# Kernel optimization log

Measured on AMD Instinct MI355X. Metric: run time of the kernel, lower is better.

## Reference

```python
import jax, jax.numpy as jnp
import numpy as np

SEQ = 4096
R_DIM = 1024
Z_DIM = 1024
AT_DIM = 1024
G_DIM = 1024


def _xavier(key, shape):
    fan_in, fan_out = shape[1], shape[0]
    limit = float(np.sqrt(6.0 / (fan_in + fan_out)))
    return jax.random.uniform(key, shape, jnp.float32, -limit, limit)


def setup_inputs() -> dict:
    key = jax.random.key(0)
    ks = jax.random.split(key, 12)
    return {
        "R": jax.random.normal(ks[0], (SEQ, R_DIM), jnp.float32),
        "W_alpha": _xavier(ks[1], (R_DIM, 2 * R_DIM)),
        "b_alpha": jnp.zeros((R_DIM,), jnp.float32),
        "W_delta": _xavier(ks[2], (R_DIM, 2 * R_DIM)),
        "b_delta": jnp.zeros((R_DIM,), jnp.float32),
        "W_q": _xavier(ks[3], (AT_DIM, Z_DIM)),
        "b_q": jnp.zeros((AT_DIM,), jnp.float32),
        "W_k": _xavier(ks[4], (AT_DIM, Z_DIM)),
        "b_k": jnp.zeros((AT_DIM,), jnp.float32),
        "W_v": _xavier(ks[5], (AT_DIM, Z_DIM)),
        "b_v": jnp.zeros((AT_DIM,), jnp.float32),
        "W_z": _xavier(ks[6], (Z_DIM, R_DIM)),
        "b_z": jnp.zeros((Z_DIM,), jnp.float32),
        "W_f": _xavier(ks[7], (AT_DIM, G_DIM)),
        "b_f": jnp.zeros((AT_DIM,), jnp.float32),
        "W_EMA": _xavier(ks[8], (G_DIM, R_DIM)),
        "b_EMA": jnp.zeros((G_DIM,), jnp.float32),
        "W_z_at": _xavier(ks[9], (G_DIM, AT_DIM)),
        "b_z_at": jnp.zeros((G_DIM,), jnp.float32),
        "W_i": _xavier(ks[10], (1, R_DIM)),
        "b_i": jnp.zeros((1,), jnp.float32),
        "W_final": _xavier(ks[11], (1, G_DIM)),
    }


def reference(R, W_alpha, b_alpha, W_delta, b_delta, W_q, b_q, W_k, b_k,
              W_v, b_v, W_z, b_z, W_f, b_f, W_EMA, b_EMA, W_z_at, b_z_at,
              W_i, b_i, W_final):
    r_dim = R.shape[-1]
    at_dim = W_q.shape[0]
    # prepend zero row; r_t / r_{t-1} pairs
    R2 = jnp.concatenate([jnp.zeros((1, r_dim), R.dtype), R], axis=0)
    r_t, r_prev = R2[1:], R2[:-1]
    concat_r = jnp.concatenate([r_prev, r_t], axis=1)  # [m, 2r]
    alpha = jnp.tanh(concat_r @ W_alpha.T + b_alpha)
    delta = jnp.tanh(concat_r @ W_delta.T + b_delta)
    R_EMA = alpha * r_t + (1.0 - alpha) * delta * r_prev
    Z = jax.nn.silu(R_EMA @ W_z.T + b_z)
    Q = Z @ W_q.T + b_q
    K = Z @ W_k.T + b_k
    V = Z @ W_v.T + b_v
    scores = (Q @ K.T) / jnp.sqrt(jnp.float32(at_dim))  # [m, m]
    weights = jax.nn.softmax(scores, axis=-1)
    Z_at = weights @ V
    R_EMA_p = R_EMA @ W_EMA.T + b_EMA
    f = jax.nn.sigmoid(R_EMA_p @ W_f.T + b_f)
    Z_at_p = f * Z_at
    Z_EMA_f = Z_at_p @ W_z_at.T + b_z_at
    Z_tp = jnp.tanh(R_EMA_p + Z_EMA_f)
    i = jnp.tanh(R_EMA @ W_i.T + b_i)  # [m, 1]
    Z_final = i * Z_tp + (1.0 - i) * R_EMA_p
    p_hat = jax.nn.sigmoid(Z_final @ W_final.T)  # [m, 1]
    return p_hat
```

## Files before the change

kernel.cpp:

```cpp
#include <hip/hip_runtime.h>
#include <cstdint>
#include <cmath>

#define MB (1024ull * 1024ull)

typedef unsigned short u16;
typedef __attribute__((ext_vector_type(8))) short short8;
typedef __attribute__((ext_vector_type(4))) float f32x4;

enum { M_TANH = 0, M_ZRE = 1, M_QKV = 2, M_SIG = 3, M_SCALE = 4, M_PVMUL = 5, M_F32 = 6 };

__device__ __forceinline__ u16 f2b(float f) {
  union { float f; uint32_t u; } v; v.f = f;
  uint32_t r = v.u + 0x7FFFu + ((v.u >> 16) & 1u);
  return (u16)(r >> 16);
}
__device__ __forceinline__ float b2f(u16 u) {
  union { uint32_t u; float f; } v; v.u = ((uint32_t)u) << 16;
  return v.f;
}

typedef __attribute__((address_space(3))) uint32_t lds_u32;
typedef const __attribute__((address_space(1))) uint32_t glb_u32;

__device__ __forceinline__ void gload16(const void* g, void* l) {
  __builtin_amdgcn_global_load_lds((glb_u32*)g, (lds_u32*)l, 16, 0, 0);
}

template <int MODE, int BNT>
__global__ __launch_bounds__(256) void gemm(const u16* __restrict__ A,
                                            const u16* __restrict__ B,
                                            const float* __restrict__ bias,
                                            const u16* __restrict__ auxb,
                                            u16* __restrict__ Cb,
                                            u16* __restrict__ Cb2,
                                            float* __restrict__ Cf,
                                            int K, int lda, int ldb, float scale) {
  constexpr int NJ = (BNT == 128) ? 4 : 2;
  __shared__ u16 As[128 * 32];
  __shared__ u16 Bs[BNT * 32];
  const int tid = threadIdx.x;
  const int wid = tid >> 6, lane = tid & 63;
  const int bm = blockIdx.y * 128, bn = blockIdx.x * BNT;
  const int wm = wid >> 1, wn = wid & 1;

  const int srow = tid >> 2;
  const int schunk = (tid & 3) ^ ((srow >> 1) & 3);
  const u16* gA = A + (size_t)(bm + srow) * lda + schunk * 8;
  const u16* gB = B + (size_t)(bn + srow) * ldb + schunk * 8;
  u16* ldsA = &As[wid * 512];
  u16* ldsB = &Bs[wid * 512];

  f32x4 acc[4][NJ];
#pragma unroll
  for (int i = 0; i < 4; ++i)
#pragma unroll
    for (int j = 0; j < NJ; ++j) acc[i][j] = (f32x4){0.f, 0.f, 0.f, 0.f};

  const int ar = lane & 15;
  const int pch = (((lane >> 4) ^ ((ar >> 1) & 3))) * 8;

  for (int k0 = 0; k0 < K; k0 += 32) {
    gload16(gA, ldsA);
    gload16(gA + (size_t)64 * lda, ldsA + 2048);
    gload16(gB, ldsB);
    if (BNT == 128) gload16(gB + (size_t)64 * ldb, ldsB + 2048);
    gA += 32; gB += 32;
    __syncthreads();
    short8 af[4], bf[NJ];
#pragma unroll
    for (int i = 0; i < 4; ++i)
      af[i] = *reinterpret_cast<const short8*>(&As[(wm * 64 + i * 16 + ar) * 32 + pch]);
#pragma unroll
    for (int j = 0; j < NJ; ++j)
      bf[j] = *reinterpret_cast<const short8*>(&Bs[(wn * (BNT / 2) + j * 16 + ar) * 32 + pch]);
#pragma unroll
    for (int i = 0; i < 4; ++i)
#pragma unroll
      for (int j = 0; j < NJ; ++j)
        acc[i][j] = __builtin_amdgcn_mfma_f32_16x16x32_bf16(af[i], bf[j], acc[i][j], 0, 0, 0);
    __syncthreads();
  }

#pragma unroll
  for (int i = 0; i < 4; ++i) {
    const int rb = bm + wm * 64 + i * 16 + (lane >> 4) * 4;
#pragma unroll
    for (int j = 0; j < NJ; ++j) {
      const int n = bn + wn * (BNT / 2) + j * 16 + (lane & 15);
#pragma unroll
      for (int r = 0; r < 4; ++r) {
        const int m = rb + r;
        float v = acc[i][j][r];
        if (MODE == M_TANH) {
          v = tanhf(v + bias[n]);
          Cb[(size_t)m * 2048 + n] = f2b(v);
        } else if (MODE == M_ZRE) {
          v += bias[n];
          if (n < 1024) { const float s = v / (1.f + expf(-v)); Cb[(size_t)m * 1024 + n] = f2b(s); }
          else Cb2[(size_t)m * 1024 + (n - 1024)] = f2b(v);
        } else if (MODE == M_QKV) {
          v += bias[n];
          if (n < 2048) Cb[(size_t)m * 2048 + n] = f2b(v);
          else Cb2[(size_t)m * 1024 + (n - 2048)] = f2b(v);
        } else if (MODE == M_SIG) {
          v = 1.f / (1.f + expf(-(v + bias[n])));
          Cb[(size_t)m * 1024 + n] = f2b(v);
        } else if (MODE == M_SCALE) {
          Cb[(size_t)m * 4096 + n] = f2b(v * scale);
        } else if (MODE == M_PVMUL) {
          v *= b2f(auxb[(size_t)m * 1024 + n]);
          Cb[(size_t)m * 1024 + n] = f2b(v);
        } else if (MODE == M_F32) {
          Cf[(size_t)m * 1024 + n] = v + bias[n];
        }
      }
    }
  }
}

__global__ __launch_bounds__(256) void convert_all(
    const float* __restrict__ s0, const float* __restrict__ s1, const float* __restrict__ s2,
    const float* __restrict__ s3, const float* __restrict__ s4, const float* __restrict__ s5,
    const float* __restrict__ s6, const float* __restrict__ s7, const float* __restrict__ s8,
    u16* __restrict__ Wad, u16* __restrict__ Wze, u16* __restrict__ Wqkv,
    u16* __restrict__ Wfb, u16* __restrict__ Wzab) {
  const int idx = blockIdx.x * 256 + threadIdx.x;
  const float* src; u16* dst; int off;
  if      (idx < 524288)  { src = s0; dst = Wad;           off = idx; }
  else if (idx < 1048576) { src = s1; dst = Wad + 2097152; off = idx - 524288; }
  else if (idx < 1310720) { src = s2; dst = Wze;           off = idx - 1048576; }
  else if (idx < 1572864) { src = s3; dst = Wze + 1048576; off = idx - 1310720; }
  else if (idx < 1835008) { src = s4; dst = Wqkv;          off = idx - 1572864; }
  else if (idx < 2097152) { src = s5; dst = Wqkv + 1048576; off = idx - 1835008; }
  else if (idx < 2359296) { src = s6; dst = Wqkv + 2097152; off = idx - 2097152; }
  else if (idx < 2621440) { src = s7; dst = Wfb;           off = idx - 2359296; }
  else                    { src = s8; dst = Wzab;          off = idx - 2621440; }
  const float4 v = reinterpret_cast<const float4*>(src)[off];
  ushort4 o; o.x = f2b(v.x); o.y = f2b(v.y); o.z = f2b(v.z); o.w = f2b(v.w);
  reinterpret_cast<ushort4*>(dst)[off] = o;
}

__global__ void copy_bias(const float* __restrict__ ba, const float* __restrict__ bd,
                          const float* __restrict__ bz, const float* __restrict__ be,
                          const float* __restrict__ bq, const float* __restrict__ bk,
                          const float* __restrict__ bv,
                          float* __restrict__ bad, float* __restrict__ bze,
                          float* __restrict__ bqkv) {
  const int t = threadIdx.x;
  const float4* src; float4* dst;
  switch (blockIdx.x) {
    case 0: src = (const float4*)ba; dst = (float4*)bad; break;
    case 1: src = (const float4*)bd; dst = (float4*)(bad + 1024); break;
    case 2: src = (const float4*)bz; dst = (float4*)bze; break;
    case 3: src = (const float4*)be; dst = (float4*)(bze + 1024); break;
    case 4: src = (const float4*)bq; dst = (float4*)bqkv; break;
    case 5: src = (const float4*)bk; dst = (float4*)(bqkv + 1024); break;
    default: src = (const float4*)bv; dst = (float4*)(bqkv + 2048); break;
  }
  dst[t] = src[t];
}

__global__ __launch_bounds__(256) void concat_kern(const float* __restrict__ R,
                                                   u16* __restrict__ Rc) {
  const int idx = blockIdx.x * 256 + threadIdx.x;
  const int m = idx >> 9;
  const int c = (idx & 511) * 4;
  float4 v;
  if (c < 1024) {
    if (m > 0) v = *reinterpret_cast<const float4*>(&R[(size_t)(m - 1) * 1024 + c]);
    else v = make_float4(0.f, 0.f, 0.f, 0.f);
  } else {
    v = *reinterpret_cast<const float4*>(&R[(size_t)m * 1024 + (c - 1024)]);
  }
  ushort4 o; o.x = f2b(v.x); o.y = f2b(v.y); o.z = f2b(v.z); o.w = f2b(v.w);
  reinterpret_cast<ushort4*>(Rc)[idx] = o;
}

__global__ __launch_bounds__(256) void ema_combine(const float* __restrict__ R,
                                                   const u16* __restrict__ adb,
                                                   u16* __restrict__ REMA) {
  const int idx = blockIdx.x * 256 + threadIdx.x;
  const int m = idx >> 8, c4 = idx & 255;
  const float4 rt = reinterpret_cast<const float4*>(R)[idx];
  float4 rp = make_float4(0.f, 0.f, 0.f, 0.f);
  if (m > 0) rp = reinterpret_cast<const float4*>(R)[idx - 256];
  const ushort4 a4 = reinterpret_cast<const ushort4*>(adb)[m * 512 + c4];
  const ushort4 d4 = reinterpret_cast<const ushort4*>(adb)[m * 512 + 256 + c4];
  ushort4 o;
  { const float av = b2f(a4.x); o.x = f2b(av * rt.x + (1.f - av) * b2f(d4.x) * rp.x); }
  { const float av = b2f(a4.y); o.y = f2b(av * rt.y + (1.f - av) * b2f(d4.y) * rp.y); }
  { const float av = b2f(a4.z); o.z = f2b(av * rt.z + (1.f - av) * b2f(d4.z) * rp.z); }
  { const float av = b2f(a4.w); o.w = f2b(av * rt.w + (1.f - av) * b2f(d4.w) * rp.w); }
  reinterpret_cast<ushort4*>(REMA)[idx] = o;
}

__device__ __forceinline__ float waveMax(float v) {
#pragma unroll
  for (int o = 32; o; o >>= 1) v = fmaxf(v, __shfl_down(v, o));
  return v;
}
__device__ __forceinline__ float waveSum(float v) {
#pragma unroll
  for (int o = 32; o; o >>= 1) v += __shfl_down(v, o);
  return v;
}

__global__ __launch_bounds__(256) void softmax_rows(u16* __restrict__ S) {
  u16* p = S + (size_t)blockIdx.x * 4096;
  const int tid = threadIdx.x;
  float v[16];
#pragma unroll
  for (int j = 0; j < 4; ++j) {
    const ushort4 t = *reinterpret_cast<const ushort4*>(&p[tid * 4 + 1024 * j]);
    v[4 * j + 0] = b2f(t.x); v[4 * j + 1] = b2f(t.y);
    v[4 * j + 2] = b2f(t.z); v[4 * j + 3] = b2f(t.w);
  }
  float mx = -INFINITY;
#pragma unroll
  for (int j = 0; j < 16; ++j) mx = fmaxf(mx, v[j]);
  __shared__ float red[4];
  const float wm = waveMax(mx);
  if ((tid & 63) == 0) red[tid >> 6] = wm;
  __syncthreads();
  mx = fmaxf(fmaxf(red[0], red[1]), fmaxf(red[2], red[3]));
  __syncthreads();
  float sum = 0.f;
#pragma unroll
  for (int j = 0; j < 16; ++j) { v[j] = expf(v[j] - mx); sum += v[j]; }
  const float ws_ = waveSum(sum);
  if ((tid & 63) == 0) red[tid >> 6] = ws_;
  __syncthreads();
  const float inv = 1.f / (red[0] + red[1] + red[2] + red[3]);
#pragma unroll
  for (int j = 0; j < 4; ++j) {
    ushort4 t;
    t.x = f2b(v[4 * j + 0] * inv); t.y = f2b(v[4 * j + 1] * inv);
    t.z = f2b(v[4 * j + 2] * inv); t.w = f2b(v[4 * j + 3] * inv);
    *reinterpret_cast<ushort4*>(&p[tid * 4 + 1024 * j]) = t;
  }
}

__global__ __launch_bounds__(256) void transpose_b16(const u16* __restrict__ V,
                                                     u16* __restrict__ Vt) {
  __shared__ u16 t[64][72];
  const int bn = blockIdx.x * 64;
  const int bk = blockIdx.y * 64;
  const int tx = threadIdx.x & 15, ty = threadIdx.x >> 4;
#pragma unroll
  for (int i = 0; i < 64; i += 16) {
    const ushort4 v = *reinterpret_cast<const ushort4*>(&V[(size_t)(bk + ty + i) * 1024 + bn + tx * 4]);
    t[ty + i][tx * 4 + 0] = v.x; t[ty + i][tx * 4 + 1] = v.y;
    t[ty + i][tx * 4 + 2] = v.z; t[ty + i][tx * 4 + 3] = v.w;
  }
  __syncthreads();
#pragma unroll
  for (int i = 0; i < 64; i += 16) {
    ushort4 w;
    w.x = t[tx * 4 + 0][ty + i]; w.y = t[tx * 4 + 1][ty + i];
    w.z = t[tx * 4 + 2][ty + i]; w.w = t[tx * 4 + 3][ty + i];
    *reinterpret_cast<ushort4*>(&Vt[(size_t)(bn + ty + i) * 4096 + bk + tx * 4]) = w;
  }
}

__global__ void rowdot_i(const u16* __restrict__ REMA, const float* __restrict__ Wi,
                         const float* __restrict__ bi, float* __restrict__ iv) {
  const int m = blockIdx.x, l = threadIdx.x;
  float s = 0.f;
#pragma unroll
  for (int j = 0; j < 16; ++j) s += b2f(REMA[(size_t)m * 1024 + l + 64 * j]) * Wi[l + 64 * j];
#pragma unroll
  for (int o = 32; o; o >>= 1) s += __shfl_down(s, o);
  if (l == 0) iv[m] = tanhf(s + bi[0]);
}

__global__ void final_kern(const u16* __restrict__ REMApb, const float* __restrict__ ZEMAf,
                           const float* __restrict__ iv, const float* __restrict__ Wfin,
                           float* __restrict__ out) {
  const int m = blockIdx.x, l = threadIdx.x;
  const float im = iv[m];
  float s = 0.f;
#pragma unroll
  for (int j = 0; j < 16; ++j) {
    const int n = l + 64 * j;
    const float rp = b2f(REMApb[(size_t)m * 1024 + n]);
    const float zf = im * tanhf(rp + ZEMAf[(size_t)m * 1024 + n]) + (1.f - im) * rp;
    s += zf * Wfin[n];
  }
#pragma unroll
  for (int o = 32; o; o >>= 1) s += __shfl_down(s, o);
  if (l == 0) out[m] = 1.f / (1.f + expf(-s));
}

extern "C" void kernel_launch(void* const* d_in, const int* in_sizes, int n_in,
                              void* d_out, int out_size, void* d_ws, size_t ws_size,
                              hipStream_t stream) {
  const float* R       = (const float*)d_in[0];
  const float* W_alpha = (const float*)d_in[1];  const float* b_alpha = (const float*)d_in[2];
  const float* W_delta = (const float*)d_in[3];  const float* b_delta = (const float*)d_in[4];
  const float* W_q     = (const float*)d_in[5];  const float* b_q     = (const float*)d_in[6];
  const float* W_k     = (const float*)d_in[7];  const float* b_k     = (const float*)d_in[8];
  const float* W_v     = (const float*)d_in[9];  const float* b_v     = (const float*)d_in[10];
  const float* W_z     = (const float*)d_in[11]; const float* b_z     = (const float*)d_in[12];
  const float* W_f     = (const float*)d_in[13]; const float* b_f     = (const float*)d_in[14];
  const float* W_EMA   = (const float*)d_in[15]; const float* b_EMA   = (const float*)d_in[16];
  const float* W_z_at  = (const float*)d_in[17]; const float* b_z_at  = (const float*)d_in[18];
  const float* W_i     = (const float*)d_in[19]; const float* b_i     = (const float*)d_in[20];
  const float* W_final = (const float*)d_in[21];
  float* out = (float*)d_out;
  uint8_t* w8 = (uint8_t*)d_ws;

  u16*   Rc     = (u16*)(w8 + 0 * MB);
  u16*   Zb     = (u16*)(w8 + 0 * MB);
  u16*   REMApb = (u16*)(w8 + 8 * MB);
  u16*   Wad    = (u16*)(w8 + 16 * MB);
  u16*   fvb    = (u16*)(w8 + 16 * MB);
  u16*   adb    = (u16*)(w8 + 24 * MB);
  float* ZEMAf  = (float*)(w8 + 24 * MB);
  u16*   Wqkv   = (u16*)(w8 + 40 * MB);
  u16*   Vtb    = (u16*)(w8 + 40 * MB);
  u16*   Wze    = (u16*)(w8 + 46 * MB);
  u16*   Wfb    = (u16*)(w8 + 50 * MB);
  u16*   Wzab   = (u16*)(w8 + 52 * MB);
  u16*   REMAb  = (u16*)(w8 + 54 * MB);
  u16*   QKb    = (u16*)(w8 + 62 * MB);
  u16*   Zatpb  = (u16*)(w8 + 62 * MB);
  u16*   Vb     = (u16*)(w8 + 78 * MB);
  u16*   Sb     = (u16*)(w8 + 78 * MB);
  float* iv     = (float*)(w8 + 110 * MB);
  float* bad    = (float*)(w8 + 110 * MB + 64 * 1024);
  float* bze    = bad + 2048;
  float* bqkv   = bze + 2048;

  const dim3 blk(256);
  convert_all<<<11264, blk, 0, stream>>>(W_alpha, W_delta, W_z, W_EMA, W_q, W_k, W_v, W_f, W_z_at,
                                         Wad, Wze, Wqkv, Wfb, Wzab);
  concat_kern<<<8192, blk, 0, stream>>>(R, Rc);
  copy_bias<<<7, blk, 0, stream>>>(b_alpha, b_delta, b_z, b_EMA, b_q, b_k, b_v, bad, bze, bqkv);

  gemm<M_TANH, 128><<<dim3(16, 32), blk, 0, stream>>>(Rc, Wad, bad, nullptr, adb, nullptr, nullptr, 2048, 2048, 2048, 1.f);
  ema_combine<<<4096, blk, 0, stream>>>(R, adb, REMAb);
  gemm<M_ZRE, 128><<<dim3(16, 32), blk, 0, stream>>>(REMAb, Wze, bze, nullptr, Zb, REMApb, nullptr, 1024, 1024, 1024, 1.f);
  gemm<M_QKV, 128><<<dim3(24, 32), blk, 0, stream>>>(Zb, Wqkv, bqkv, nullptr, QKb, Vb, nullptr, 1024, 1024, 1024, 1.f);
  gemm<M_SIG, 64><<<dim3(16, 32), blk, 0, stream>>>(REMApb, Wfb, b_f, nullptr, fvb, nullptr, nullptr, 1024, 1024, 1024, 1.f);
  transpose_b16<<<dim3(16, 64), blk, 0, stream>>>(Vb, Vtb);
  gemm<M_SCALE, 128><<<dim3(32, 32), blk, 0, stream>>>(QKb, QKb + 1024, nullptr, nullptr, Sb, nullptr, nullptr, 1024, 2048, 2048, 0.03125f);
  softmax_rows<<<4096, blk, 0, stream>>>(Sb);
  gemm<M_PVMUL, 64><<<dim3(16, 32), blk, 0, stream>>>(Sb, Vtb, nullptr, fvb, Zatpb, nullptr, nullptr, 4096, 4096, 4096, 1.f);
  gemm<M_F32, 64><<<dim3(16, 32), blk, 0, stream>>>(Zatpb, Wzab, b_z_at, nullptr, nullptr, nullptr, ZEMAf, 1024, 1024, 1024, 1.f);
  rowdot_i<<<4096, 64, 0, stream>>>(REMAb, W_i, b_i, iv);
  final_kern<<<4096, 64, 0, stream>>>(REMApb, ZEMAf, iv, W_final, out);
}
```

Before: 370.1 us.

## Double-buffer GEMM LDS tiles, remap workgroups across XCDs, fuse i-gate into final kernel

The GEMM main loop now ping-pongs between two LDS buffers, issuing the global-to-LDS loads for the next K tile before computing the current one. This drops one barrier per iteration and overlaps load latency with MFMA work. Workgroup IDs are remapped in chunks of 8 so neighbouring tiles land on the same XCD for better L2 reuse. The rowdot_i kernel is folded into final_kern using an xor-shuffle reduction, which removes a launch and the iv buffer. The cost is doubled LDS per block, which may reduce occupancy.

```diff
diff --git a/kernel.cpp b/kernel.cpp
--- a/kernel.cpp
+++ b/kernel.cpp
@@ -37,19 +37,21 @@
                                             float* __restrict__ Cf,
                                             int K, int lda, int ldb, float scale) {
   constexpr int NJ = (BNT == 128) ? 4 : 2;
-  __shared__ u16 As[128 * 32];
-  __shared__ u16 Bs[BNT * 32];
+  __shared__ u16 As[2][128 * 32];
+  __shared__ u16 Bs[2][BNT * 32];
   const int tid = threadIdx.x;
   const int wid = tid >> 6, lane = tid & 63;
-  const int bm = blockIdx.y * 128, bn = blockIdx.x * BNT;
+
+  const int gx = gridDim.x, nwg = gx * gridDim.y;
+  int id = blockIdx.y * gx + blockIdx.x;
+  if ((nwg & 7) == 0) id = (id & 7) * (nwg >> 3) + (id >> 3);
+  const int bm = (id / gx) * 128, bn = (id % gx) * BNT;
   const int wm = wid >> 1, wn = wid & 1;
 
   const int srow = tid >> 2;
   const int schunk = (tid & 3) ^ ((srow >> 1) & 3);
   const u16* gA = A + (size_t)(bm + srow) * lda + schunk * 8;
   const u16* gB = B + (size_t)(bn + srow) * ldb + schunk * 8;
-  u16* ldsA = &As[wid * 512];
-  u16* ldsB = &Bs[wid * 512];
 
   f32x4 acc[4][NJ];
 #pragma unroll
@@ -60,26 +62,36 @@
   const int ar = lane & 15;
   const int pch = (((lane >> 4) ^ ((ar >> 1) & 3))) * 8;
 
-  for (int k0 = 0; k0 < K; k0 += 32) {
-    gload16(gA, ldsA);
-    gload16(gA + (size_t)64 * lda, ldsA + 2048);
-    gload16(gB, ldsB);
-    if (BNT == 128) gload16(gB + (size_t)64 * ldb, ldsB + 2048);
-    gA += 32; gB += 32;
-    __syncthreads();
+  const int NT = K >> 5;
+
+  auto stage = [&](int buf, int t) {
+    const u16* a = gA + (size_t)t * 32;
+    const u16* b = gB + (size_t)t * 32;
+    gload16(a, &As[buf][wid * 512]);
+    gload16(a + (size_t)64 * lda, &As[buf][wid * 512 + 2048]);
+    gload16(b, &Bs[buf][wid * 512]);
+    if (BNT == 128) gload16(b + (size_t)64 * ldb, &Bs[buf][wid * 512 + 2048]);
+  };
+
+  stage(0, 0);
+  __syncthreads();
+  int cur = 0;
+  for (int t = 0; t < NT; ++t) {
+    if (t + 1 < NT) stage(cur ^ 1, t + 1);
     short8 af[4], bf[NJ];
 #pragma unroll
     for (int i = 0; i < 4; ++i)
-      af[i] = *reinterpret_cast<const short8*>(&As[(wm * 64 + i * 16 + ar) * 32 + pch]);
+      af[i] = *reinterpret_cast<const short8*>(&As[cur][(wm * 64 + i * 16 + ar) * 32 + pch]);
 #pragma unroll
     for (int j = 0; j < NJ; ++j)
-      bf[j] = *reinterpret_cast<const short8*>(&Bs[(wn * (BNT / 2) + j * 16 + ar) * 32 + pch]);
+      bf[j] = *reinterpret_cast<const short8*>(&Bs[cur][(wn * (BNT / 2) + j * 16 + ar) * 32 + pch]);
 #pragma unroll
     for (int i = 0; i < 4; ++i)
 #pragma unroll
       for (int j = 0; j < NJ; ++j)
         acc[i][j] = __builtin_amdgcn_mfma_f32_16x16x32_bf16(af[i], bf[j], acc[i][j], 0, 0, 0);
     __syncthreads();
+    cur ^= 1;
   }
 
 #pragma unroll
@@ -263,22 +275,20 @@
   }
 }
 
-__global__ void rowdot_i(const u16* __restrict__ REMA, const float* __restrict__ Wi,
-                         const float* __restrict__ bi, float* __restrict__ iv) {
+__global__ void final_kern(const u16* __restrict__ REMAb, const u16* __restrict__ REMApb,
+                           const float* __restrict__ ZEMAf,
+                           const float* __restrict__ Wi, const float* __restrict__ bi,
+                           const float* __restrict__ Wfin, float* __restrict__ out) {
   const int m = blockIdx.x, l = threadIdx.x;
-  float s = 0.f;
-#pragma unroll
-  for (int j = 0; j < 16; ++j) s += b2f(REMA[(size_t)m * 1024 + l + 64 * j]) * Wi[l + 64 * j];
-#pragma unroll
-  for (int o = 32; o; o >>= 1) s += __shfl_down(s, o);
-  if (l == 0) iv[m] = tanhf(s + bi[0]);
-}
-
-__global__ void final_kern(const u16* __restrict__ REMApb, const float* __restrict__ ZEMAf,
-                           const float* __restrict__ iv, const float* __restrict__ Wfin,
-                           float* __restrict__ out) {
-  const int m = blockIdx.x, l = threadIdx.x;
-  const float im = iv[m];
+  float si = 0.f;
+#pragma unroll
+  for (int j = 0; j < 16; ++j) {
+    const int n = l + 64 * j;
+    si += b2f(REMAb[(size_t)m * 1024 + n]) * Wi[n];
+  }
+#pragma unroll
+  for (int o = 32; o; o >>= 1) si += __shfl_xor(si, o);
+  const float im = tanhf(si + bi[0]);
   float s = 0.f;
 #pragma unroll
   for (int j = 0; j < 16; ++j) {
@@ -327,7 +337,6 @@
   u16*   Zatpb  = (u16*)(w8 + 62 * MB);
   u16*   Vb     = (u16*)(w8 + 78 * MB);
   u16*   Sb     = (u16*)(w8 + 78 * MB);
-  float* iv     = (float*)(w8 + 110 * MB);
   float* bad    = (float*)(w8 + 110 * MB + 64 * 1024);
   float* bze    = bad + 2048;
   float* bqkv   = bze + 2048;
@@ -348,6 +357,5 @@
   softmax_rows<<<4096, blk, 0, stream>>>(Sb);
   gemm<M_PVMUL, 64><<<dim3(16, 32), blk, 0, stream>>>(Sb, Vtb, nullptr, fvb, Zatpb, nullptr, nullptr, 4096, 4096, 4096, 1.f);
   gemm<M_F32, 64><<<dim3(16, 32), blk, 0, stream>>>(Zatpb, Wzab, b_z_at, nullptr, nullptr, nullptr, ZEMAf, 1024, 1024, 1024, 1.f);
-  rowdot_i<<<4096, 64, 0, stream>>>(REMAb, W_i, b_i, iv);
-  final_kern<<<4096, 64, 0, stream>>>(REMApb, ZEMAf, iv, W_final, out);
-}
+  final_kern<<<4096, 64, 0, stream>>>(REMAb, REMApb, ZEMAf, W_i, b_i, W_final, out);
+}
```

Result: faster. 345.6 us (-6.6%).
